# Performance work log

Measured on AMD Instinct MI355X. Metric: run time of the kernel, lower is better.

## Reference

```python
import jax, jax.numpy as jnp
import numpy as np

N = 1048576
DIM = 2
HID = 64
E = 4


def setup_inputs() -> dict:
    key = jax.random.key(0)
    ks = jax.random.split(key, 10)
    s_in = 1.0 / np.sqrt(DIM)
    s_hid = 1.0 / np.sqrt(HID)
    return {
        "x": jax.random.normal(ks[0], (N, DIM), dtype=jnp.float32),
        # router: Linear(dim -> E)
        "rW": jax.random.uniform(ks[1], (DIM, E), minval=-s_in, maxval=s_in, dtype=jnp.float32),
        "rb": jax.random.uniform(ks[2], (E,), minval=-s_in, maxval=s_in, dtype=jnp.float32),
        # stacked expert weights: Linear(dim->hid), Linear(hid->hid), Linear(hid->dim)
        "w1": jax.random.uniform(ks[3], (E, DIM, HID), minval=-s_in, maxval=s_in, dtype=jnp.float32),
        "b1": jax.random.uniform(ks[4], (E, HID), minval=-s_in, maxval=s_in, dtype=jnp.float32),
        "w2": jax.random.uniform(ks[5], (E, HID, HID), minval=-s_hid, maxval=s_hid, dtype=jnp.float32),
        "b2": jax.random.uniform(ks[6], (E, HID), minval=-s_hid, maxval=s_hid, dtype=jnp.float32),
        "w3": jax.random.uniform(ks[7], (E, HID, DIM), minval=-s_hid, maxval=s_hid, dtype=jnp.float32),
        "b3": jax.random.uniform(ks[8], (E, DIM), minval=-s_hid, maxval=s_hid, dtype=jnp.float32),
    }


def reference(x, rW, rb, w1, b1, w2, b2, w3, b3):
    # Router: hard top-1 via argmax, exactly as torch.argmax(router_logits, -1)
    router_logits = x @ rW + rb                       # [N, E]
    best = jnp.argmax(router_logits, axis=-1)         # [N]

    # Compute all experts densely (vectorized replacement of the masked loop),
    # then select the winning expert's output per token via one-hot.
    h = jax.nn.relu(jnp.einsum('nd,edh->enh', x, w1) + b1[:, None, :])   # [E, N, HID]
    h = jax.nn.relu(jnp.einsum('enh,ehk->enk', h, w2) + b2[:, None, :])  # [E, N, HID]
    y = jnp.einsum('enh,ehd->end', h, w3) + b3[:, None, :]               # [E, N, DIM]

    onehot = jax.nn.one_hot(best, E, dtype=x.dtype)   # [N, E]
    out = jnp.einsum('end,ne->nd', y, onehot)         # [N, DIM]
    return out, router_logits
```

## Files before the change

kernel.cpp:

```cpp
#include <hip/hip_runtime.h>

#define NTOK 1048576
#define HID 64
#define TPB 256
#define TPB_TOK 2048
#define RPT (TPB_TOK / TPB)
#define NBLK (NTOK / TPB_TOK)
#define MAXSLOT (TPB_TOK + 64)
#define MAXTILE (TPB_TOK / 16 + 4)

typedef _Float16 half8 __attribute__((ext_vector_type(8)));
typedef float f32x4 __attribute__((ext_vector_type(4)));

__global__ void prep_w2_frag(const float* __restrict__ w2, _Float16* __restrict__ wsf) {
    int idx  = blockIdx.x * 256 + threadIdx.x;
    int j    = idx & 7;
    int lane = (idx >> 3) & 63;
    int ks   = (idx >> 9) & 1;
    int mt   = (idx >> 10) & 3;
    int e    = idx >> 12;
    int kin  = ks * 32 + (lane >> 4) * 8 + j;
    int m    = mt * 16 + (lane & 15);
    wsf[idx] = (_Float16)w2[(e * HID + kin) * HID + m];
}

__global__ __launch_bounds__(TPB, 2) void moe_kernel(
    const float* __restrict__ x, const float* __restrict__ rW, const float* __restrict__ rb,
    const float* __restrict__ w1, const float* __restrict__ b1,
    const float* __restrict__ b2,
    const float* __restrict__ w3, const float* __restrict__ b3,
    const _Float16* __restrict__ wsf, float* __restrict__ out)
{
    __shared__ float2 xs[MAXSLOT];
    __shared__ int ids[MAXSLOT];
    __shared__ int wcnt[4][4];
    __shared__ int seg_start[4], cnt_sh[4], cumt[5];
    __shared__ unsigned tmap[MAXTILE];

    const int t = threadIdx.x, w = t >> 6, lane = t & 63;
    const int base = blockIdx.x * TPB_TOK;
    const unsigned long long lt = (1ull << lane) - 1ull;

    const float r00 = rW[0], r01 = rW[1], r02 = rW[2], r03 = rW[3];
    const float r10 = rW[4], r11 = rW[5], r12 = rW[6], r13 = rW[7];
    const float rb0 = rb[0], rb1 = rb[1], rb2 = rb[2], rb3 = rb[3];

    int c0 = 0, c1 = 0, c2 = 0, c3 = 0;
    int slotl[RPT]; int bestl[RPT]; float2 xv_[RPT];
    float* logits_out = out + 2 * NTOK;
    #pragma unroll
    for (int i = 0; i < RPT; i++) {
        int tok = base + i * TPB + t;
        float2 xv = ((const float2*)x)[tok];
        float l0 = xv.x * r00 + xv.y * r10 + rb0;
        float l1 = xv.x * r01 + xv.y * r11 + rb1;
        float l2 = xv.x * r02 + xv.y * r12 + rb2;
        float l3 = xv.x * r03 + xv.y * r13 + rb3;
        ((float4*)logits_out)[tok] = make_float4(l0, l1, l2, l3);
        int b = 0; float bv = l0;
        if (l1 > bv) { bv = l1; b = 1; }
        if (l2 > bv) { bv = l2; b = 2; }
        if (l3 > bv) { bv = l3; b = 3; }
        unsigned long long m0 = __ballot(b == 0), m1 = __ballot(b == 1),
                           m2 = __ballot(b == 2), m3 = __ballot(b == 3);
        unsigned long long mym = (b == 0) ? m0 : (b == 1) ? m1 : (b == 2) ? m2 : m3;
        int cb = (b == 0) ? c0 : (b == 1) ? c1 : (b == 2) ? c2 : c3;
        slotl[i] = cb + __popcll(mym & lt);
        bestl[i] = b; xv_[i] = xv;
        c0 += __popcll(m0); c1 += __popcll(m1); c2 += __popcll(m2); c3 += __popcll(m3);
    }
    if (lane < 4) wcnt[w][lane] = (lane == 0) ? c0 : (lane == 1) ? c1 : (lane == 2) ? c2 : c3;
    __syncthreads();
    if (t == 0) {
        int run = 0, ct = 0; cumt[0] = 0;
        for (int e = 0; e < 4; e++) {
            int c = wcnt[0][e] + wcnt[1][e] + wcnt[2][e] + wcnt[3][e];
            cnt_sh[e] = c; seg_start[e] = run;
            run += (c + 15) & ~15; ct += (c + 15) >> 4; cumt[e + 1] = ct;
        }
    }
    __syncthreads();
    int wo0 = 0, wo1 = 0, wo2 = 0, wo3 = 0;
    for (int ww = 0; ww < w; ww++) {
        wo0 += wcnt[ww][0]; wo1 += wcnt[ww][1]; wo2 += wcnt[ww][2]; wo3 += wcnt[ww][3];
    }
    #pragma unroll
    for (int i = 0; i < RPT; i++) {
        int b = bestl[i];
        int wo = (b == 0) ? wo0 : (b == 1) ? wo1 : (b == 2) ? wo2 : wo3;
        int slot = seg_start[b] + wo + slotl[i];
        xs[slot] = xv_[i];
        ids[slot] = base + i * TPB + t;
    }
    int T = cumt[4];
    for (int g = t; g < T; g += TPB) {
        int e = (g >= cumt[1]) + (g >= cumt[2]) + (g >= cumt[3]);
        int i = g - cumt[e];
        int row = seg_start[e] + 16 * i;
        int cn = cnt_sh[e] - 16 * i; if (cn > 16) cn = 16;
        tmap[g] = (unsigned)e | ((unsigned)row << 2) | ((unsigned)cn << 18);
    }
    __syncthreads();

    const int q = lane >> 4, n16 = lane & 15;
    int chunk = (T + 3) >> 2;
    int g0 = w * chunk, g1 = g0 + chunk; if (g1 > T) g1 = T;

    float w1r0[16], w1r1[16], b1r[16];
    half8 w2A[4][2];
    float4 b2r[4], w3a[4], w3b[4];
    float2 b3r = make_float2(0.f, 0.f);
    int cur_e = -1;

    for (int g = g0; g < g1; g++) {
        unsigned tm = tmap[g];
        int e   = tm & 3;
        int row = (tm >> 2) & 0xFFF;
        int cn  = tm >> 18;
        if (e != cur_e) {
            cur_e = e;
            const float* p0 = w1 + e * 128 + q * 8;
            const float* p1 = w1 + e * 128 + 64 + q * 8;
            const float* pb = b1 + e * 64 + q * 8;
            #pragma unroll
            for (int j = 0; j < 8; j++) {
                w1r0[j] = p0[j];  w1r0[8 + j] = p0[32 + j];
                w1r1[j] = p1[j];  w1r1[8 + j] = p1[32 + j];
                b1r[j]  = pb[j];  b1r[8 + j]  = pb[32 + j];
            }
            #pragma unroll
            for (int mt = 0; mt < 4; mt++) {
                w2A[mt][0] = ((const half8*)wsf)[((e * 4 + mt) * 2 + 0) * 64 + lane];
                w2A[mt][1] = ((const half8*)wsf)[((e * 4 + mt) * 2 + 1) * 64 + lane];
                b2r[mt] = ((const float4*)(b2 + e * 64))[mt * 4 + q];
                w3a[mt] = ((const float4*)(w3 + e * 128))[mt * 8 + q * 2];
                w3b[mt] = ((const float4*)(w3 + e * 128))[mt * 8 + q * 2 + 1];
            }
            b3r = ((const float2*)b3)[e];
        }
        float2 xv = xs[row + n16];
        half8 bf0, bf1;
        #pragma unroll
        for (int j = 0; j < 8; j++) {
            float ha = fmaf(xv.y, w1r1[j],     fmaf(xv.x, w1r0[j],     b1r[j]));
            float hb = fmaf(xv.y, w1r1[8 + j], fmaf(xv.x, w1r0[8 + j], b1r[8 + j]));
            bf0[j] = (_Float16)fmaxf(ha, 0.f);
            bf1[j] = (_Float16)fmaxf(hb, 0.f);
        }
        float y0 = 0.f, y1 = 0.f;
        #pragma unroll
        for (int mt = 0; mt < 4; mt++) {
            f32x4 acc = {0.f, 0.f, 0.f, 0.f};
            acc = __builtin_amdgcn_mfma_f32_16x16x32_f16(w2A[mt][0], bf0, acc, 0, 0, 0);
            acc = __builtin_amdgcn_mfma_f32_16x16x32_f16(w2A[mt][1], bf1, acc, 0, 0, 0);
            float4 bb = b2r[mt], wa = w3a[mt], wb = w3b[mt];
            float h;
            h = fmaxf(acc[0] + bb.x, 0.f); y0 = fmaf(h, wa.x, y0); y1 = fmaf(h, wa.y, y1);
            h = fmaxf(acc[1] + bb.y, 0.f); y0 = fmaf(h, wa.z, y0); y1 = fmaf(h, wa.w, y1);
            h = fmaxf(acc[2] + bb.z, 0.f); y0 = fmaf(h, wb.x, y0); y1 = fmaf(h, wb.y, y1);
            h = fmaxf(acc[3] + bb.w, 0.f); y0 = fmaf(h, wb.z, y0); y1 = fmaf(h, wb.w, y1);
        }
        y0 += __shfl_xor(y0, 16); y0 += __shfl_xor(y0, 32);
        y1 += __shfl_xor(y1, 16); y1 += __shfl_xor(y1, 32);
        if (q == 0 && n16 < cn) {
            int tok = ids[row + n16];
            ((float2*)out)[tok] = make_float2(y0 + b3r.x, y1 + b3r.y);
        }
    }
}

extern "C" void kernel_launch(void* const* d_in, const int* in_sizes, int n_in,
                              void* d_out, int out_size, void* d_ws, size_t ws_size,
                              hipStream_t stream) {
    const float* x  = (const float*)d_in[0];
    const float* rW = (const float*)d_in[1];
    const float* rb = (const float*)d_in[2];
    const float* w1 = (const float*)d_in[3];
    const float* b1 = (const float*)d_in[4];
    const float* w2 = (const float*)d_in[5];
    const float* b2 = (const float*)d_in[6];
    const float* w3 = (const float*)d_in[7];
    const float* b3 = (const float*)d_in[8];
    float* out = (float*)d_out;
    _Float16* wsf = (_Float16*)d_ws;

    hipLaunchKernelGGL(prep_w2_frag, dim3(64), dim3(256), 0, stream, w2, wsf);
    hipLaunchKernelGGL(moe_kernel, dim3(NBLK), dim3(TPB), 0, stream,
                       x, rW, rb, w1, b1, b2, w3, b3, (const _Float16*)wsf, out);
}
```

Measured before the change: 107.3 us.

## Compute first layer in packed fp16, prefetch next tile, split output accumulators

The first expert layer now runs in packed half2 arithmetic with fp16 weights, replacing fp32 FMAs and per-element conversions. The next tile's map entry, input and token id are prefetched from shared memory one iteration ahead to hide LDS latency. The layer-3 dot products use independent per-tile accumulators, which shortens the dependency chain after each MFMA. The packed fp16 layer-1 arithmetic lowers precision of the hidden activations and adds register pressure from the prefetch.

```diff
diff --git a/kernel.cpp b/kernel.cpp
--- a/kernel.cpp
+++ b/kernel.cpp
@@ -10,7 +10,12 @@
 #define MAXTILE (TPB_TOK / 16 + 4)
 
 typedef _Float16 half8 __attribute__((ext_vector_type(8)));
+typedef _Float16 half2v __attribute__((ext_vector_type(2)));
 typedef float f32x4 __attribute__((ext_vector_type(4)));
+
+static __device__ __forceinline__ half2v pkh(float a, float b) {
+    return __builtin_bit_cast(half2v, __builtin_amdgcn_cvt_pkrtz(a, b));
+}
 
 __global__ void prep_w2_frag(const float* __restrict__ w2, _Float16* __restrict__ wsf) {
     int idx  = blockIdx.x * 256 + threadIdx.x;
@@ -106,27 +111,49 @@
     int chunk = (T + 3) >> 2;
     int g0 = w * chunk, g1 = g0 + chunk; if (g1 > T) g1 = T;
 
-    float w1r0[16], w1r1[16], b1r[16];
+    half2v w1h0[8], w1h1[8], b1h[8];
     half8 w2A[4][2];
     float4 b2r[4], w3a[4], w3b[4];
     float2 b3r = make_float2(0.f, 0.f);
     int cur_e = -1;
 
+    unsigned tm_n = 0; float2 xv_n = make_float2(0.f, 0.f); int id_n = 0;
+    if (g0 < g1) {
+        tm_n = tmap[g0];
+        int r_ = (tm_n >> 2) & 0xFFF;
+        xv_n = xs[r_ + n16];
+        id_n = ids[r_ + n16];
+    }
+
     for (int g = g0; g < g1; g++) {
-        unsigned tm = tmap[g];
-        int e   = tm & 3;
-        int row = (tm >> 2) & 0xFFF;
-        int cn  = tm >> 18;
+        unsigned tm = tm_n; float2 xv = xv_n; int idv = id_n;
+        if (g + 1 < g1) {
+            tm_n = tmap[g + 1];
+            int r_ = (tm_n >> 2) & 0xFFF;
+            xv_n = xs[r_ + n16];
+            id_n = ids[r_ + n16];
+        }
+        int e  = tm & 3;
+        int cn = tm >> 18;
         if (e != cur_e) {
             cur_e = e;
-            const float* p0 = w1 + e * 128 + q * 8;
-            const float* p1 = w1 + e * 128 + 64 + q * 8;
-            const float* pb = b1 + e * 64 + q * 8;
+            const float* base0 = w1 + e * 128;
+            const float* base1 = w1 + e * 128 + 64;
+            const float* baseb = b1 + e * 64;
             #pragma unroll
-            for (int j = 0; j < 8; j++) {
-                w1r0[j] = p0[j];  w1r0[8 + j] = p0[32 + j];
-                w1r1[j] = p1[j];  w1r1[8 + j] = p1[32 + j];
-                b1r[j]  = pb[j];  b1r[8 + j]  = pb[32 + j];
+            for (int p = 0; p < 4; p++) {
+                float2 a0 = *(const float2*)(base0 + q * 8 + 2 * p);
+                float2 a1 = *(const float2*)(base0 + 32 + q * 8 + 2 * p);
+                w1h0[p]     = pkh(a0.x, a0.y);
+                w1h0[4 + p] = pkh(a1.x, a1.y);
+                float2 c0_ = *(const float2*)(base1 + q * 8 + 2 * p);
+                float2 c1_ = *(const float2*)(base1 + 32 + q * 8 + 2 * p);
+                w1h1[p]     = pkh(c0_.x, c0_.y);
+                w1h1[4 + p] = pkh(c1_.x, c1_.y);
+                float2 d0 = *(const float2*)(baseb + q * 8 + 2 * p);
+                float2 d1 = *(const float2*)(baseb + 32 + q * 8 + 2 * p);
+                b1h[p]     = pkh(d0.x, d0.y);
+                b1h[4 + p] = pkh(d1.x, d1.y);
             }
             #pragma unroll
             for (int mt = 0; mt < 4; mt++) {
@@ -138,33 +165,39 @@
             }
             b3r = ((const float2*)b3)[e];
         }
-        float2 xv = xs[row + n16];
+        half2v xh0 = pkh(xv.x, xv.x);
+        half2v xh1 = pkh(xv.y, xv.y);
+        const half2v hz = { (_Float16)0, (_Float16)0 };
         half8 bf0, bf1;
         #pragma unroll
-        for (int j = 0; j < 8; j++) {
-            float ha = fmaf(xv.y, w1r1[j],     fmaf(xv.x, w1r0[j],     b1r[j]));
-            float hb = fmaf(xv.y, w1r1[8 + j], fmaf(xv.x, w1r0[8 + j], b1r[8 + j]));
-            bf0[j] = (_Float16)fmaxf(ha, 0.f);
-            bf1[j] = (_Float16)fmaxf(hb, 0.f);
-        }
-        float y0 = 0.f, y1 = 0.f;
+        for (int p = 0; p < 4; p++) {
+            half2v ha = w1h0[p] * xh0 + w1h1[p] * xh1 + b1h[p];
+            half2v hb = w1h0[4 + p] * xh0 + w1h1[4 + p] * xh1 + b1h[4 + p];
+            ha = __builtin_elementwise_max(ha, hz);
+            hb = __builtin_elementwise_max(hb, hz);
+            bf0[2 * p] = ha.x; bf0[2 * p + 1] = ha.y;
+            bf1[2 * p] = hb.x; bf1[2 * p + 1] = hb.y;
+        }
+        float y0m[4], y1m[4];
         #pragma unroll
         for (int mt = 0; mt < 4; mt++) {
             f32x4 acc = {0.f, 0.f, 0.f, 0.f};
             acc = __builtin_amdgcn_mfma_f32_16x16x32_f16(w2A[mt][0], bf0, acc, 0, 0, 0);
             acc = __builtin_amdgcn_mfma_f32_16x16x32_f16(w2A[mt][1], bf1, acc, 0, 0, 0);
             float4 bb = b2r[mt], wa = w3a[mt], wb = w3b[mt];
-            float h;
-            h = fmaxf(acc[0] + bb.x, 0.f); y0 = fmaf(h, wa.x, y0); y1 = fmaf(h, wa.y, y1);
-            h = fmaxf(acc[1] + bb.y, 0.f); y0 = fmaf(h, wa.z, y0); y1 = fmaf(h, wa.w, y1);
-            h = fmaxf(acc[2] + bb.z, 0.f); y0 = fmaf(h, wb.x, y0); y1 = fmaf(h, wb.y, y1);
-            h = fmaxf(acc[3] + bb.w, 0.f); y0 = fmaf(h, wb.z, y0); y1 = fmaf(h, wb.w, y1);
-        }
+            float h, a0 = 0.f, a1 = 0.f;
+            h = fmaxf(acc[0] + bb.x, 0.f); a0 = fmaf(h, wa.x, a0); a1 = fmaf(h, wa.y, a1);
+            h = fmaxf(acc[1] + bb.y, 0.f); a0 = fmaf(h, wa.z, a0); a1 = fmaf(h, wa.w, a1);
+            h = fmaxf(acc[2] + bb.z, 0.f); a0 = fmaf(h, wb.x, a0); a1 = fmaf(h, wb.y, a1);
+            h = fmaxf(acc[3] + bb.w, 0.f); a0 = fmaf(h, wb.z, a0); a1 = fmaf(h, wb.w, a1);
+            y0m[mt] = a0; y1m[mt] = a1;
+        }
+        float y0 = (y0m[0] + y0m[1]) + (y0m[2] + y0m[3]);
+        float y1 = (y1m[0] + y1m[1]) + (y1m[2] + y1m[3]);
         y0 += __shfl_xor(y0, 16); y0 += __shfl_xor(y0, 32);
         y1 += __shfl_xor(y1, 16); y1 += __shfl_xor(y1, 32);
         if (q == 0 && n16 < cn) {
-            int tok = ids[row + n16];
-            ((float2*)out)[tok] = make_float2(y0 + b3r.x, y1 + b3r.y);
+            ((float2*)out)[idv] = make_float2(y0 + b3r.x, y1 + b3r.y);
         }
     }
 }
```

After: 106.0 us. Within noise of the previous version (-1.3%).
